# Kernel tuning notes

Measured on AMD Instinct MI355X. Metric: run time of the kernel, lower is better.

Reference implementation:

```python
import jax, jax.numpy as jnp
import numpy as np

L = (7, 5, 5, 5, 5)            # num_quantized_values (all odd -> exact product codebook)
LATENT_DIM = len(L)
MAX_SEQ_LEN = 2048
LATENT_SEQ_LEN = 1024
CODEBOOK_SIZE = int(np.prod(L))  # 4375


def build_codebook():
    # Matches build_codebook_recursive: dim 0 varies slowest ('ij' meshgrid + ravel).
    ranges = [jnp.arange(-(l // 2), l // 2 + 1, dtype=jnp.int32) for l in L]
    grids = jnp.meshgrid(*ranges, indexing='ij')
    return jnp.stack([g.ravel() for g in grids], axis=-1)  # [K, D] int32


def setup_inputs() -> dict:
    key = jax.random.key(0)
    k1, k2, k3 = jax.random.split(key, 3)
    B, S, D = 16, MAX_SEQ_LEN, 1024
    x = jax.random.normal(k1, (B, S, D), dtype=jnp.float32)
    W_enc = jax.random.normal(k2, (D, LATENT_DIM), dtype=jnp.float32) / np.sqrt(D)
    W_dec = jax.random.normal(k3, (LATENT_DIM, D), dtype=jnp.float32) / np.sqrt(LATENT_DIM)
    return {"x": x, "W_enc": W_enc, "W_dec": W_dec}


def reference(x, W_enc, W_dec):
    B, S, _ = x.shape
    codebook = build_codebook()                                   # [K, D_lat]
    half = jnp.array([l // 2 for l in L], dtype=jnp.float32)      # (L/2).int()

    # encode: stand-in linear encoder, then zero tokens past latent_seq_len
    h = jnp.einsum('bsd,de->bse', x, W_enc)                        # [B,S,D_lat]
    mask = (jnp.arange(S) < LATENT_SEQ_LEN)[None, :, None]
    h = h * mask
    z_e = h.reshape(-1, LATENT_DIM)                                # [N, D_lat]

    # quantize: FSQ tanh squash + round with straight-through estimator
    z_e_sq = half * jnp.tanh(z_e)
    z_q = jnp.round(z_e_sq)
    z = jax.lax.stop_gradient(z_q - z_e_sq) + z_e_sq

    # brute-force codebook index lookup: [N,1,D] == [K,D] -> all -> argmax
    matches = jnp.all(z.astype(jnp.int32)[:, None, :] == codebook[None], axis=-1)  # [N,K]
    idx = jnp.argmax(matches, axis=1)                              # [N]

    # codebook usage (fresh zero-initialized usage buffer)
    used = jnp.zeros((CODEBOOK_SIZE,), dtype=jnp.float32).at[idx].set(1.0)
    unique = jnp.sum(used)
    usage = (unique + (CODEBOOK_SIZE - unique) * jnp.exp(jnp.float32(-1.0))) / CODEBOOK_SIZE

    # decode: stand-in linear decoder
    z3 = z.reshape(-1, MAX_SEQ_LEN, LATENT_DIM)                    # [B, num_latents, D_lat]
    x_out = jnp.einsum('bse,ed->bsd', z3, W_dec)                   # [B,S,D]
    percent_masked = jnp.float32(0.0)

    return x_out, z_e, z_q, usage, unique.astype(jnp.int32), percent_masked
```

## Files before the change

### kernel.cpp

```cpp
#include <hip/hip_runtime.h>

#define MAX_SEQ   2048
#define LAT_SEQ   1024
#define DIM       1024
#define DLAT      5
#define K_CB      4375
#define ZERO_IDX  2187

typedef float vf4 __attribute__((ext_vector_type(4)));

__device__ __forceinline__ void nt_store4(float* p, vf4 v) {
    __builtin_nontemporal_store(v, (vf4*)p);
}

__global__ __launch_bounds__(256) void fsq_main(
    const float* __restrict__ x,
    const float* __restrict__ Wenc,
    const float* __restrict__ Wdec,
    float* __restrict__ xout,
    float* __restrict__ ze,
    float* __restrict__ zq)
{
    __shared__ float wencT[DLAT * DIM];

    const int tid  = threadIdx.x;
    const int wave = tid >> 6;
    const int lane = tid & 63;
    const int u0   = (blockIdx.x * 4 + wave) * 2;

    int t[2];  long long row[2], rowm[2];
    #pragma unroll
    for (int p = 0; p < 2; ++p) {
        const int u = u0 + p;
        const int b = u >> 10, s = u & 1023;
        t[p]    = b * MAX_SEQ + s;
        row[p]  = (long long)t[p] * DIM;
        rowm[p] = row[p] + (long long)LAT_SEQ * DIM;
    }

    float4 v[2][4];
    #pragma unroll
    for (int p = 0; p < 2; ++p)
        #pragma unroll
        for (int q = 0; q < 4; ++q)
            v[p][q] = *(const float4*)(x + row[p] + q * 256 + lane * 4);

    const vf4 z4 = {0.f, 0.f, 0.f, 0.f};
    #pragma unroll
    for (int p = 0; p < 2; ++p) {
        #pragma unroll
        for (int q = 0; q < 4; ++q)
            nt_store4(xout + rowm[p] + q * 256 + lane * 4, z4);
        if (lane < DLAT) {
            const int tm = t[p] + LAT_SEQ;
            ze[tm * DLAT + lane] = 0.f;
            zq[tm * DLAT + lane] = 0.f;
        }
    }

    #pragma unroll
    for (int m = 0; m < 20; ++m) {
        const int k = tid + 256 * m;
        const int e = k >> 10, d = k & 1023;
        wencT[k] = Wenc[d * DLAT + e];
    }
    __syncthreads();

    float acc[2][DLAT] = {};
    #pragma unroll
    for (int q = 0; q < 4; ++q) {
        const int c0 = q * 256 + lane * 4;
        #pragma unroll
        for (int e = 0; e < DLAT; ++e) {
            const float4 w = *(const float4*)(wencT + e * DIM + c0);
            #pragma unroll
            for (int p = 0; p < 2; ++p)
                acc[p][e] += v[p][q].x * w.x + v[p][q].y * w.y
                           + v[p][q].z * w.z + v[p][q].w * w.w;
        }
    }
    #pragma unroll
    for (int p = 0; p < 2; ++p)
        #pragma unroll
        for (int e = 0; e < DLAT; ++e) {
            float a = acc[p][e];
            #pragma unroll
            for (int o = 32; o > 0; o >>= 1) a += __shfl_xor(a, o, 64);
            acc[p][e] = a;
        }

    const float halfv[DLAT] = {3.f, 2.f, 2.f, 2.f, 2.f};
    float zqv[2][DLAT];
    #pragma unroll
    for (int p = 0; p < 2; ++p) {
        #pragma unroll
        for (int e = 0; e < DLAT; ++e)
            zqv[p][e] = rintf(halfv[e] * tanhf(acc[p][e]));
        if (lane < DLAT) {
            ze[t[p] * DLAT + lane] = acc[p][lane];
            zq[t[p] * DLAT + lane] = zqv[p][lane];
        }
    }

    #pragma unroll
    for (int q = 0; q < 4; ++q) {
        const int c0 = q * 256 + lane * 4;
        float4 w[DLAT];
        #pragma unroll
        for (int e = 0; e < DLAT; ++e)
            w[e] = *(const float4*)(Wdec + e * DIM + c0);
        #pragma unroll
        for (int p = 0; p < 2; ++p) {
            vf4 o = {0.f, 0.f, 0.f, 0.f};
            #pragma unroll
            for (int e = 0; e < DLAT; ++e) {
                o.x += zqv[p][e] * w[e].x; o.y += zqv[p][e] * w[e].y;
                o.z += zqv[p][e] * w[e].z; o.w += zqv[p][e] * w[e].w;
            }
            nt_store4(xout + row[p] + c0, o);
        }
    }
}

__global__ __launch_bounds__(1024) void finalize(
    const float* __restrict__ zq, float* __restrict__ scal)
{
    __shared__ unsigned char bm[K_CB];
    __shared__ int sh[16];
    const int tid = threadIdx.x;

    for (int i = tid; i < K_CB; i += 1024) bm[i] = 0;
    __syncthreads();

    for (int u = tid; u < 16384; u += 1024) {
        const int t = (u >> 10) * MAX_SEQ + (u & 1023);
        const float* z = zq + (long long)t * DLAT;
        const int c0 = (int)z[0], c1 = (int)z[1], c2 = (int)z[2],
                  c3 = (int)z[3], c4 = (int)z[4];
        const int idx = ((((c0 + 3) * 5 + (c1 + 2)) * 5 + (c2 + 2)) * 5
                          + (c3 + 2)) * 5 + (c4 + 2);
        bm[idx] = 1;
    }
    __syncthreads();
    if (tid == 0) bm[ZERO_IDX] = 1;
    __syncthreads();

    int sum = 0;
    for (int i = tid; i < K_CB; i += 1024) sum += bm[i];
    #pragma unroll
    for (int o = 32; o > 0; o >>= 1) sum += __shfl_xor(sum, o, 64);
    if ((tid & 63) == 0) sh[tid >> 6] = sum;
    __syncthreads();
    if (tid == 0) {
        int tot = 0;
        #pragma unroll
        for (int wv = 0; wv < 16; ++wv) tot += sh[wv];
        const float uniq  = (float)tot;
        const float usage = (uniq + ((float)K_CB - uniq) * expf(-1.0f)) / (float)K_CB;
        scal[0] = usage;
        scal[1] = uniq;
        scal[2] = 0.0f;
    }
}

extern "C" void kernel_launch(void* const* d_in, const int* in_sizes, int n_in,
                              void* d_out, int out_size, void* d_ws, size_t ws_size,
                              hipStream_t stream) {
    const float* x    = (const float*)d_in[0];
    const float* Wenc = (const float*)d_in[1];
    const float* Wdec = (const float*)d_in[2];

    float* out  = (float*)d_out;
    float* xout = out;
    float* ze   = out + 33554432;
    float* zq   = ze + 163840;
    float* scal = zq + 163840;

    (void)d_ws; (void)ws_size;

    fsq_main<<<2048, 256, 0, stream>>>(x, Wenc, Wdec, xout, ze, zq);
    finalize<<<1, 1024, 0, stream>>>(zq, scal);
}
```

Baseline: 40.60 us.

## Split zero-fill of masked rows into dedicated fill blocks

Result: slower. 42.44 us (+4.5%).

```diff
diff --git a/kernel.cpp b/kernel.cpp
--- a/kernel.cpp
+++ b/kernel.cpp
@@ -6,10 +6,12 @@
 #define DLAT      5
 #define K_CB      4375
 #define ZERO_IDX  2187
+#define FILLB     512
+#define COMPB     2048
 
 typedef float vf4 __attribute__((ext_vector_type(4)));
 
-__device__ __forceinline__ void nt_store4(float* p, vf4 v) {
+__device__ __forceinline__ void nt_store4(float4* p, vf4 v) {
     __builtin_nontemporal_store(v, (vf4*)p);
 }
 
@@ -23,19 +25,40 @@
 {
     __shared__ float wencT[DLAT * DIM];
 
-    const int tid  = threadIdx.x;
+    const int tid = threadIdx.x;
+
+    if (blockIdx.x < FILLB) {
+        const vf4 z4 = {0.f, 0.f, 0.f, 0.f};
+        const int tg = blockIdx.x * 256 + tid;
+        float4* xo4 = (float4*)xout;
+        #pragma unroll
+        for (int k = 0; k < 32; ++k) {
+            const int g   = tg + k * (FILLB * 256);
+            const int b16 = g >> 18;
+            const int off = g & 262143;
+            nt_store4(xo4 + (long long)b16 * 524288 + 262144 + off, z4);
+        }
+        if (tg < 20480) {
+            const int b16 = tg / 1280;
+            const int off = tg - b16 * 1280;
+            const long long idx = (long long)b16 * 2560 + 1280 + off;
+            nt_store4((float4*)ze + idx, z4);
+            nt_store4((float4*)zq + idx, z4);
+        }
+        return;
+    }
+
     const int wave = tid >> 6;
     const int lane = tid & 63;
-    const int u0   = (blockIdx.x * 4 + wave) * 2;
+    const int u0   = ((blockIdx.x - FILLB) * 4 + wave) * 2;
 
-    int t[2];  long long row[2], rowm[2];
+    int t[2];  long long row[2];
     #pragma unroll
     for (int p = 0; p < 2; ++p) {
         const int u = u0 + p;
         const int b = u >> 10, s = u & 1023;
-        t[p]    = b * MAX_SEQ + s;
-        row[p]  = (long long)t[p] * DIM;
-        rowm[p] = row[p] + (long long)LAT_SEQ * DIM;
+        t[p]   = b * MAX_SEQ + s;
+        row[p] = (long long)t[p] * DIM;
     }
 
     float4 v[2][4];
@@ -44,19 +67,6 @@
         #pragma unroll
         for (int q = 0; q < 4; ++q)
             v[p][q] = *(const float4*)(x + row[p] + q * 256 + lane * 4);
-
-    const vf4 z4 = {0.f, 0.f, 0.f, 0.f};
-    #pragma unroll
-    for (int p = 0; p < 2; ++p) {
-        #pragma unroll
-        for (int q = 0; q < 4; ++q)
-            nt_store4(xout + rowm[p] + q * 256 + lane * 4, z4);
-        if (lane < DLAT) {
-            const int tm = t[p] + LAT_SEQ;
-            ze[tm * DLAT + lane] = 0.f;
-            zq[tm * DLAT + lane] = 0.f;
-        }
-    }
 
     #pragma unroll
     for (int m = 0; m < 20; ++m) {
@@ -117,7 +127,7 @@
                 o.x += zqv[p][e] * w[e].x; o.y += zqv[p][e] * w[e].y;
                 o.z += zqv[p][e] * w[e].z; o.w += zqv[p][e] * w[e].w;
             }
-            nt_store4(xout + row[p] + c0, o);
+            nt_store4((float4*)(xout + row[p] + c0), o);
         }
     }
 }
@@ -178,6 +188,6 @@
 
     (void)d_ws; (void)ws_size;
 
-    fsq_main<<<2048, 256, 0, stream>>>(x, Wenc, Wdec, xout, ze, zq);
+    fsq_main<<<FILLB + COMPB, 256, 0, stream>>>(x, Wenc, Wdec, xout, ze, zq);
     finalize<<<1, 1024, 0, stream>>>(zq, scal);
 }
```
